# Kernel tuning notes

Hardware: AMD Instinct MI355X
Metric: run time of the kernel (lower is better)

## Reference

```python
import jax, jax.numpy as jnp
import numpy as np

TOPK_INC = 20  # top-k vertices per mention that form a hyperedge (torch.topk(attention_a, 20))
TOPK_OUT = 2   # top-k node reps concatenated into the output (torch.topk(X_score, k=2))


def _indicator_from_rows(att, idx):
    # att: [N, N], idx: [A] int. Rows with idx == 0 are skipped, as in the original loop.
    N = att.shape[0]
    rows = att[idx]                                   # [A, N] gather of attention rows
    _, top = jax.lax.top_k(rows, TOPK_INC)            # [A, TOPK_INC]
    mask = (idx != 0).astype(att.dtype)               # [A]
    vals = jnp.broadcast_to(mask[:, None], top.shape).reshape(-1)
    # scatter-max builds the 0/1 incidence vector (multiple mentions OR together)
    return jnp.zeros((N,), att.dtype).at[top.reshape(-1)].max(vals)  # [N]


def _forward_one(h, att, a_idx, b_idx, spk, W_w, W_b, S_w, S_b):
    # h: [N, H], att: [N, N], spk: [N] (single speaker row since speak_num == 1 -> E = 3)
    a_ind = _indicator_from_rows(att, a_idx)
    b_ind = _indicator_from_rows(att, b_idx)
    Hyper0 = jnp.stack([a_ind, b_ind, spk], axis=0)   # [E, N] binary incidence
    Dv = 1.0 / jnp.sqrt(Hyper0.sum(axis=0) + 1.0)     # sqrt(inverse(diag(Dv) + I)) diagonal, [N]
    De = 1.0 / jnp.sqrt(Hyper0.sum(axis=1))           # sqrt(inverse(diag(De))) diagonal, [E]
    Hyper = Hyper0 @ att                              # [E, N]  (dropout is identity in eval)
    Hyper_att = jax.nn.softmax(Hyper, axis=-1)        # F.softmax over last dim for 2D input
    Hyper_prime = Hyper_att @ h                       # [E, H]
    w = jax.nn.softmax(Hyper_prime @ W_w.T + W_b, axis=0)[:, 0]  # [E]
    # A = diag(Dv) @ Hyper0.T @ diag(w) @ diag(De) @ Hyper @ diag(Dv); X = A @ h.
    # Associate as M @ (K @ h) to avoid materializing the [N, N] matrix A.
    K = (w * De)[:, None] * Hyper * Dv[None, :]       # [E, N]
    M = Hyper0.T * Dv[:, None]                        # [N, E]
    X = M @ (K @ h)                                   # [N, H]
    score = (X @ S_w.T + S_b)[:, 0]                   # [N]
    _, top = jax.lax.top_k(score, TOPK_OUT)           # [2]
    return X[top].reshape(-1)                         # [2*H]


def setup_inputs() -> dict:
    key = jax.random.key(0)
    B, N, H, A = 32, 1024, 768, 8
    ks = jax.random.split(key, 8)
    inp = jax.random.normal(ks[0], (B, N, H), dtype=jnp.float32)
    word_att = jax.random.uniform(ks[1], (B, 1, N, N), dtype=jnp.float32)
    a_idx = jax.random.randint(ks[2], (B, A), 0, N)
    b_idx = jax.random.randint(ks[3], (B, A), 0, N)
    speak_num = jnp.ones((B, 1), dtype=jnp.int64 if jax.config.jax_enable_x64 else jnp.int32)
    speak_all = jax.random.randint(ks[4], (B, 3, N), 0, 2).astype(jnp.float32)
    W_w = jax.random.normal(ks[5], (1, H), dtype=jnp.float32) * (1.0 / np.sqrt(H))
    W_b = jnp.zeros((1,), dtype=jnp.float32)
    score_w = jax.random.normal(ks[6], (1, H), dtype=jnp.float32) * (1.0 / np.sqrt(H))
    score_b = jnp.zeros((1,), dtype=jnp.float32)
    return {"input": inp, "word_att": word_att, "a_idx": a_idx, "b_idx": b_idx,
            "speak_num": speak_num, "speak_all": speak_all,
            "W_w": W_w, "W_b": W_b, "score_w": score_w, "score_b": score_b}


def reference(input, word_att, a_idx, b_idx, speak_num, speak_all, W_w, W_b, score_w, score_b):
    # speak_num is all ones by construction -> exactly one speaker hyperedge per sample (E = 3)
    att = word_att[:, 0]           # [B, N, N]
    spk = speak_all[:, 0]          # [B, N]
    f = jax.vmap(_forward_one, in_axes=(0, 0, 0, 0, 0, None, None, None, None))
    return f(input, att, a_idx, b_idx, spk, W_w, W_b, score_w, score_b)  # [B, 2*H]
```

## Files before the change

### kernel.cpp

```cpp
#include <hip/hip_runtime.h>
#include <math.h>

#define B_ 32
#define N_ 1024
#define H_ 768
#define A_ 8
#define TOPK_ 20
#define CH4_ 32
#define CMAX_ 1280

__device__ __forceinline__ float wsum(float x) {
#pragma unroll
    for (int off = 32; off > 0; off >>= 1) x += __shfl_xor(x, off);
    return x;
}

__global__ __launch_bounds__(1024) void k1_ind(
    const float* __restrict__ att, const int* __restrict__ a_idx,
    const int* __restrict__ b_idx, const float* __restrict__ speak_all,
    float* __restrict__ aind, float* __restrict__ bind,
    float* __restrict__ Dv, float* __restrict__ De,
    float4* __restrict__ comp, int* __restrict__ npadArr)
{
    const int b = blockIdx.x;
    const int tid = threadIdx.x;
    const int w = tid >> 6, lane = tid & 63;
    __shared__ float s_ind[2][N_];
    __shared__ float s_red[3][16];
    __shared__ int wcnt[16];
    __shared__ int woff[17];

    s_ind[0][tid] = 0.f;
    s_ind[1][tid] = 0.f;
    __syncthreads();

    const int which = w >> 3;
    const int r = w & 7;
    const int idx = which ? b_idx[b * A_ + r] : a_idx[b * A_ + r];
    if (idx != 0) {
        const float* row = att + ((size_t)b * N_ + idx) * N_;
        float v[16];
#pragma unroll
        for (int k = 0; k < 16; ++k) v[k] = row[(k << 6) + lane];
        float* dst = s_ind[which];
        for (int t = 0; t < TOPK_; ++t) {
            float bv = v[0]; int bk = 0;
#pragma unroll
            for (int k = 1; k < 16; ++k)
                if (v[k] > bv) { bv = v[k]; bk = k; }
            int bc = (bk << 6) + lane;
#pragma unroll
            for (int off = 32; off > 0; off >>= 1) {
                float ov = __shfl_xor(bv, off);
                int oc = __shfl_xor(bc, off);
                if (ov > bv || (ov == bv && oc < bc)) { bv = ov; bc = oc; }
            }
            if (lane == 0) dst[bc] = 1.f;
            if (lane == (bc & 63)) v[bc >> 6] = -INFINITY;
        }
    }
    __syncthreads();

    const float sa = s_ind[0][tid], sb = s_ind[1][tid];
    const float ss = speak_all[(size_t)b * 3 * N_ + tid];
    aind[b * N_ + tid] = sa;
    bind[b * N_ + tid] = sb;
    Dv[b * N_ + tid] = 1.f / sqrtf(sa + sb + ss + 1.f);

    float p[3] = {sa, sb, ss};
#pragma unroll
    for (int e = 0; e < 3; ++e) {
        float x = wsum(p[e]);
        if (lane == 0) s_red[e][w] = x;
    }

    const bool act = (sa + sb + ss) > 0.f;
    const unsigned long long m = __ballot(act);
    const int wrank = (int)__popcll(m & ((1ull << lane) - 1ull));
    if (lane == 0) wcnt[w] = (int)__popcll(m);
    __syncthreads();
    if (tid == 0) {
        int s = 0;
        for (int i = 0; i < 16; ++i) { woff[i] = s; s += wcnt[i]; }
        woff[16] = s;
        npadArr[b] = (s + 255) & ~255;
    }
    if (tid < 3) {
        float s = 0.f;
        for (int i = 0; i < 16; ++i) s += s_red[tid][i];
        De[b * 3 + tid] = 1.f / sqrtf(s);
    }
    __syncthreads();
    const int nact = woff[16];
    const int npad = (nact + 255) & ~255;
    if (act)
        comp[(size_t)b * CMAX_ + woff[w] + wrank] = make_float4(__int_as_float(tid), sa, sb, ss);
    for (int i = nact + tid; i < npad; i += 1024)
        comp[(size_t)b * CMAX_ + i] = make_float4(__int_as_float(0), 0.f, 0.f, 0.f);
}

__global__ __launch_bounds__(256, 2) void k2_hyper(
    const float* __restrict__ att, const float4* __restrict__ comp,
    const int* __restrict__ npadArr, float* __restrict__ Hyper)
{
    const int b = blockIdx.y;
    const int col0 = blockIdx.x * 32;
    const int t = threadIdx.x;
    const int cx = t & 7, ig = t >> 3;
    __shared__ float4 scomp[1024];
    __shared__ float scr[256 * 13];

    const int npad = npadArr[b];
    for (int i = t; i < npad; i += 256) scomp[i] = comp[(size_t)b * CMAX_ + i];
    __syncthreads();

    float a0x=0,a0y=0,a0z=0,a0w=0, a1x=0,a1y=0,a1z=0,a1w=0, a2x=0,a2y=0,a2z=0,a2w=0;
    const float* bb = att + (size_t)b * N_ * N_ + col0 + cx * 4;

    if (npad > 0) {
        float4 v[8], cw[8];
        int i = ig;
#pragma unroll
        for (int k = 0; k < 8; ++k) {
            const float4 c = scomp[i];
            cw[k] = c;
            v[k] = *(const float4*)(bb + (size_t)__float_as_int(c.x) * N_);
            i += 32;
        }
        while (i < npad) {
#pragma unroll
            for (int k = 0; k < 8; ++k) {
                const float4 cur = v[k];
                const float4 cc = cw[k];
                const float4 nc = scomp[i];
                cw[k] = nc;
                v[k] = *(const float4*)(bb + (size_t)__float_as_int(nc.x) * N_);
                a0x += cc.y*cur.x; a0y += cc.y*cur.y; a0z += cc.y*cur.z; a0w += cc.y*cur.w;
                a1x += cc.z*cur.x; a1y += cc.z*cur.y; a1z += cc.z*cur.z; a1w += cc.z*cur.w;
                a2x += cc.w*cur.x; a2y += cc.w*cur.y; a2z += cc.w*cur.z; a2w += cc.w*cur.w;
                i += 32;
            }
        }
#pragma unroll
        for (int k = 0; k < 8; ++k) {
            const float4 cur = v[k];
            const float4 cc = cw[k];
            a0x += cc.y*cur.x; a0y += cc.y*cur.y; a0z += cc.y*cur.z; a0w += cc.y*cur.w;
            a1x += cc.z*cur.x; a1y += cc.z*cur.y; a1z += cc.z*cur.z; a1w += cc.z*cur.w;
            a2x += cc.w*cur.x; a2y += cc.w*cur.y; a2z += cc.w*cur.z; a2w += cc.w*cur.w;
        }
    }
    __syncthreads();

    float vals[12] = {a0x,a0y,a0z,a0w, a1x,a1y,a1z,a1w, a2x,a2y,a2z,a2w};
#pragma unroll
    for (int k = 0; k < 12; ++k) scr[t * 13 + k] = vals[k];
    __syncthreads();
    for (int s = 16; s > 0; s >>= 1) {
        if (ig < s) {
#pragma unroll
            for (int k = 0; k < 12; ++k)
                scr[t * 13 + k] += scr[(t + s * 8) * 13 + k];
        }
        __syncthreads();
    }
    if (ig == 0) {
#pragma unroll
        for (int e = 0; e < 3; ++e)
#pragma unroll
            for (int j = 0; j < 4; ++j)
                Hyper[(size_t)(b * 3 + e) * N_ + col0 + cx * 4 + j] = scr[t * 13 + e * 4 + j];
    }
}

__global__ __launch_bounds__(192, 2) void k4_ug(
    const float* __restrict__ h, const float* __restrict__ Hyper,
    const float* __restrict__ Dv, float* __restrict__ UGpart)
{
    const int b = blockIdx.y, c = blockIdx.x;
    const int n0 = c * 32;
    const int t = threadIdx.x;
    const int wv = t >> 6, lane = t & 63;
    __shared__ float sH[3 * N_];
    __shared__ float sw6[6][32];
    __shared__ float smz[6];

    for (int i = t; i < 3 * N_ / 4; i += 192)
        ((float4*)sH)[i] = ((const float4*)(Hyper + (size_t)b * 3 * N_))[i];
    __syncthreads();

    {
        const float* He = sH + wv * N_;
        float m = -INFINITY;
        for (int n = lane; n < N_; n += 64) m = fmaxf(m, He[n]);
#pragma unroll
        for (int off = 32; off > 0; off >>= 1) m = fmaxf(m, __shfl_xor(m, off));
        float z = 0.f;
        for (int n = lane; n < N_; n += 64) z += expf(He[n] - m);
        z = wsum(z);
        if (lane == 0) { smz[wv] = m; smz[3 + wv] = 1.f / z; }
    }
    __syncthreads();
    if (t < 96) {
        const int e = t >> 5, r = t & 31;
        const float Hv = sH[e * N_ + n0 + r];
        sw6[e][r] = expf(Hv - smz[e]) * smz[3 + e];
        sw6[3 + e][r] = Hv * Dv[b * N_ + n0 + r];
    }
    __syncthreads();

    float u0x=0,u0y=0,u0z=0,u0w=0, u1x=0,u1y=0,u1z=0,u1w=0, u2x=0,u2y=0,u2z=0,u2w=0;
    float g0x=0,g0y=0,g0z=0,g0w=0, g1x=0,g1y=0,g1z=0,g1w=0, g2x=0,g2y=0,g2z=0,g2w=0;
    const float* base = h + (size_t)b * N_ * H_ + (size_t)n0 * H_ + t * 4;

    float4 v[8];
#pragma unroll
    for (int k = 0; k < 8; ++k) v[k] = *(const float4*)(base + (size_t)k * H_);
#pragma unroll
    for (int r8 = 0; r8 < 32; r8 += 8) {
#pragma unroll
        for (int k = 0; k < 8; ++k) {
            const int r = r8 + k;
            const float4 cur = v[k];
            if (r + 8 < 32) v[k] = *(const float4*)(base + (size_t)(r + 8) * H_);
            const float w0 = sw6[0][r], w1 = sw6[1][r], w2 = sw6[2][r];
            const float g0 = sw6[3][r], g1 = sw6[4][r], g2 = sw6[5][r];
            u0x += w0*cur.x; u0y += w0*cur.y; u0z += w0*cur.z; u0w += w0*cur.w;
            u1x += w1*cur.x; u1y += w1*cur.y; u1z += w1*cur.z; u1w += w1*cur.w;
            u2x += w2*cur.x; u2y += w2*cur.y; u2z += w2*cur.z; u2w += w2*cur.w;
            g0x += g0*cur.x; g0y += g0*cur.y; g0z += g0*cur.z; g0w += g0*cur.w;
            g1x += g1*cur.x; g1y += g1*cur.y; g1z += g1*cur.z; g1w += g1*cur.w;
            g2x += g2*cur.x; g2y += g2*cur.y; g2z += g2*cur.z; g2w += g2*cur.w;
        }
    }
    float* up = UGpart + (size_t)(b * CH4_ + c) * 6 * H_ + t * 4;
    *(float4*)(up)          = make_float4(u0x, u0y, u0z, u0w);
    *(float4*)(up + H_)     = make_float4(u1x, u1y, u1z, u1w);
    *(float4*)(up + 2*H_)   = make_float4(u2x, u2y, u2z, u2w);
    *(float4*)(up + 3*H_)   = make_float4(g0x, g0y, g0z, g0w);
    *(float4*)(up + 4*H_)   = make_float4(g1x, g1y, g1z, g1w);
    *(float4*)(up + 5*H_)   = make_float4(g2x, g2y, g2z, g2w);
}

__global__ __launch_bounds__(256, 2) void k4b_red(
    const float* __restrict__ UGpart, float* __restrict__ U, float* __restrict__ G)
{
    const int gid = blockIdx.x * 256 + threadIdx.x;
    const int b = gid / 1152;
    const int rem = gid % 1152;
    const int s = rem / 192;
    const int col = (rem % 192) * 4;

    const float* p = UGpart + (size_t)b * CH4_ * 6 * H_ + s * H_ + col;
    float4 a0 = make_float4(0,0,0,0), a1 = make_float4(0,0,0,0);
    float4 a2 = make_float4(0,0,0,0), a3 = make_float4(0,0,0,0);
#pragma unroll
    for (int c = 0; c < CH4_; c += 4) {
        const float4 v0 = *(const float4*)(p + (size_t)(c + 0) * 6 * H_);
        const float4 v1 = *(const float4*)(p + (size_t)(c + 1) * 6 * H_);
        const float4 v2 = *(const float4*)(p + (size_t)(c + 2) * 6 * H_);
        const float4 v3 = *(const float4*)(p + (size_t)(c + 3) * 6 * H_);
        a0.x += v0.x; a0.y += v0.y; a0.z += v0.z; a0.w += v0.w;
        a1.x += v1.x; a1.y += v1.y; a1.z += v1.z; a1.w += v1.w;
        a2.x += v2.x; a2.y += v2.y; a2.z += v2.z; a2.w += v2.w;
        a3.x += v3.x; a3.y += v3.y; a3.z += v3.z; a3.w += v3.w;
    }
    const float4 acc = make_float4(a0.x+a1.x+a2.x+a3.x, a0.y+a1.y+a2.y+a3.y,
                                   a0.z+a1.z+a2.z+a3.z, a0.w+a1.w+a2.w+a3.w);
    if (s < 3) *(float4*)(U + ((size_t)(b * 3 + s)) * H_ + col) = acc;
    else       *(float4*)(G + ((size_t)(b * 3 + s - 3)) * H_ + col) = acc;
}

__global__ __launch_bounds__(256) void k5_fin(
    const float* __restrict__ U, const float* __restrict__ G,
    const float* __restrict__ De, const float* __restrict__ Dv,
    const float* __restrict__ aind, const float* __restrict__ bind,
    const float* __restrict__ speak_all,
    const float* __restrict__ W_w, const float* __restrict__ W_b,
    const float* __restrict__ S_w, const float* __restrict__ S_b,
    float* __restrict__ out)
{
    const int b = blockIdx.x, tid = threadIdx.x;
    const int lane = tid & 63, wv = tid >> 6;
    __shared__ float sKh[3 * H_];
    __shared__ float sscore[N_];
    __shared__ float sred[16];
    __shared__ int sidx[4];

    const float* Ub = U + (size_t)b * 3 * H_;
    const float* Gb = G + (size_t)b * 3 * H_;

    float p0 = 0.f, p1 = 0.f, p2 = 0.f;
    for (int j = tid; j < H_; j += 256) {
        const float ww = W_w[j];
        p0 += Ub[j] * ww; p1 += Ub[H_ + j] * ww; p2 += Ub[2 * H_ + j] * ww;
    }
    p0 = wsum(p0); p1 = wsum(p1); p2 = wsum(p2);
    if (lane == 0) { sred[wv * 3 + 0] = p0; sred[wv * 3 + 1] = p1; sred[wv * 3 + 2] = p2; }
    __syncthreads();
    const float wb = W_b[0];
    const float l0 = sred[0] + sred[3] + sred[6] + sred[9]  + wb;
    const float l1 = sred[1] + sred[4] + sred[7] + sred[10] + wb;
    const float l2 = sred[2] + sred[5] + sred[8] + sred[11] + wb;
    const float mx = fmaxf(l0, fmaxf(l1, l2));
    const float e0 = expf(l0 - mx), e1 = expf(l1 - mx), e2 = expf(l2 - mx);
    const float inv = 1.f / (e0 + e1 + e2);
    const float wd0 = e0 * inv * De[b * 3 + 0];
    const float wd1 = e1 * inv * De[b * 3 + 1];
    const float wd2 = e2 * inv * De[b * 3 + 2];
    __syncthreads();

    for (int j = tid; j < H_; j += 256) {
        sKh[j]          = wd0 * Gb[j];
        sKh[H_ + j]     = wd1 * Gb[H_ + j];
        sKh[2 * H_ + j] = wd2 * Gb[2 * H_ + j];
    }
    __syncthreads();

    float q0 = 0.f, q1 = 0.f, q2 = 0.f;
    for (int j = tid; j < H_; j += 256) {
        const float sw2 = S_w[j];
        q0 += sKh[j] * sw2; q1 += sKh[H_ + j] * sw2; q2 += sKh[2 * H_ + j] * sw2;
    }
    q0 = wsum(q0); q1 = wsum(q1); q2 = wsum(q2);
    if (lane == 0) { sred[wv * 3 + 0] = q0; sred[wv * 3 + 1] = q1; sred[wv * 3 + 2] = q2; }
    __syncthreads();
    q0 = sred[0] + sred[3] + sred[6] + sred[9];
    q1 = sred[1] + sred[4] + sred[7] + sred[10];
    q2 = sred[2] + sred[5] + sred[8] + sred[11];

    const float sb0 = S_b[0];
    const float* av = aind + b * N_;
    const float* bv2 = bind + b * N_;
    const float* dv = Dv + b * N_;
    const float* sv = speak_all + (size_t)b * 3 * N_;
    for (int n = tid; n < N_; n += 256)
        sscore[n] = dv[n] * (av[n] * q0 + bv2[n] * q1 + sv[n] * q2) + sb0;
    __syncthreads();

    int r0;
    {
        float best = -INFINITY; int bi = N_;
        for (int n = tid; n < N_; n += 256) {
            const float s = sscore[n];
            if (s > best || (s == best && n < bi)) { best = s; bi = n; }
        }
#pragma unroll
        for (int off = 32; off > 0; off >>= 1) {
            const float ov = __shfl_xor(best, off); const int oi = __shfl_xor(bi, off);
            if (ov > best || (ov == best && oi < bi)) { best = ov; bi = oi; }
        }
        if (lane == 0) { sred[wv] = best; sidx[wv] = bi; }
        __syncthreads();
        float v = -INFINITY; int i = N_;
        for (int k = 0; k < 4; ++k)
            if (sred[k] > v || (sred[k] == v && sidx[k] < i)) { v = sred[k]; i = sidx[k]; }
        r0 = i;
    }
    __syncthreads();
    int r1;
    {
        float best = -INFINITY; int bi = N_;
        for (int n = tid; n < N_; n += 256) {
            if (n == r0) continue;
            const float s = sscore[n];
            if (s > best || (s == best && n < bi)) { best = s; bi = n; }
        }
#pragma unroll
        for (int off = 32; off > 0; off >>= 1) {
            const float ov = __shfl_xor(best, off); const int oi = __shfl_xor(bi, off);
            if (ov > best || (ov == best && oi < bi)) { best = ov; bi = oi; }
        }
        if (lane == 0) { sred[wv] = best; sidx[wv] = bi; }
        __syncthreads();
        float v = -INFINITY; int i = N_;
        for (int k = 0; k < 4; ++k)
            if (sred[k] > v || (sred[k] == v && sidx[k] < i)) { v = sred[k]; i = sidx[k]; }
        r1 = i;
    }

    float* ob = out + (size_t)b * 2 * H_;
    {
        const float d = dv[r0], wa = av[r0], wbn = bv2[r0], wsv = sv[r0];
        for (int j = tid; j < H_; j += 256)
            ob[j] = d * (wa * sKh[j] + wbn * sKh[H_ + j] + wsv * sKh[2 * H_ + j]);
    }
    {
        const float d = dv[r1], wa = av[r1], wbn = bv2[r1], wsv = sv[r1];
        for (int j = tid; j < H_; j += 256)
            ob[H_ + j] = d * (wa * sKh[j] + wbn * sKh[H_ + j] + wsv * sKh[2 * H_ + j]);
    }
}

extern "C" void kernel_launch(void* const* d_in, const int* in_sizes, int n_in,
                              void* d_out, int out_size, void* d_ws, size_t ws_size,
                              hipStream_t stream)
{
    const float* h         = (const float*)d_in[0];
    const float* att       = (const float*)d_in[1];
    const int*   a_idx     = (const int*)d_in[2];
    const int*   b_idx     = (const int*)d_in[3];
    const float* speak_all = (const float*)d_in[5];
    const float* W_w       = (const float*)d_in[6];
    const float* W_b       = (const float*)d_in[7];
    const float* S_w       = (const float*)d_in[8];
    const float* S_b       = (const float*)d_in[9];
    float* out = (float*)d_out;

    float* ws      = (float*)d_ws;
    float* aind    = ws;
    float* bind    = aind + B_ * N_;
    float* Dv      = bind + B_ * N_;
    float* De      = Dv + B_ * N_;
    int*   npadArr = (int*)(De + 128);
    float4* comp   = (float4*)(De + 256);
    float* Hyper   = De + 256 + B_ * CMAX_ * 4;
    float* UGpart  = Hyper + B_ * 3 * N_;
    float* U       = UGpart + (size_t)B_ * CH4_ * 6 * H_;
    float* G       = U + B_ * 3 * H_;

    k1_ind<<<B_, 1024, 0, stream>>>(att, a_idx, b_idx, speak_all, aind, bind, Dv, De, comp, npadArr);
    k2_hyper<<<dim3(32, B_), 256, 0, stream>>>(att, comp, npadArr, Hyper);
    k4_ug<<<dim3(CH4_, B_), 192, 0, stream>>>(h, Hyper, Dv, UGpart);
    k4b_red<<<144, 256, 0, stream>>>(UGpart, U, G);
    k5_fin<<<B_, 256, 0, stream>>>(U, G, De, Dv, aind, bind, speak_all, W_w, W_b, S_w, S_b, out);
}
```

Measured before the change: 82.96 us.

## Fuse Hyper and UG kernels with per-batch atomic barrier, fold reduction into final

Merges the Hyper gather-matvec kernel and the softmax/h-projection kernel into one launch. The 32 blocks of each batch sync through a global atomic counter with spin-wait, so Hyper is computed and consumed in a single kernel. The partial-sum reduction kernel is folded into the final kernel, which reduces UGpart into shared memory. This removes two kernel launches and the U/G round trip. The costs are a simpler non-prefetched gather loop, float3 loads of h, and a spin barrier that relies on all 1024 blocks being co-resident (256 threads, up to 4 per CU), otherwise it can deadlock.

```diff
diff --git a/kernel.cpp b/kernel.cpp
--- a/kernel.cpp
+++ b/kernel.cpp
@@ -6,7 +6,7 @@
 #define H_ 768
 #define A_ 8
 #define TOPK_ 20
-#define CH4_ 32
+#define CH_ 32
 #define CMAX_ 1280
 
 __device__ __forceinline__ float wsum(float x) {
@@ -20,7 +20,7 @@
     const int* __restrict__ b_idx, const float* __restrict__ speak_all,
     float* __restrict__ aind, float* __restrict__ bind,
     float* __restrict__ Dv, float* __restrict__ De,
-    float4* __restrict__ comp, int* __restrict__ npadArr)
+    float4* __restrict__ comp, int* __restrict__ npadArr, int* __restrict__ cnt)
 {
     const int b = blockIdx.x;
     const int tid = threadIdx.x;
@@ -30,6 +30,8 @@
     __shared__ int wcnt[16];
     __shared__ int woff[17];
 
+    if (b == 0 && tid < 64) cnt[tid] = 0;
+
     s_ind[0][tid] = 0.f;
     s_ind[1][tid] = 0.f;
     __syncthreads();
@@ -43,7 +45,7 @@
 #pragma unroll
         for (int k = 0; k < 16; ++k) v[k] = row[(k << 6) + lane];
         float* dst = s_ind[which];
-        for (int t = 0; t < TOPK_; ++t) {
+        for (int t2 = 0; t2 < TOPK_; ++t2) {
             float bv = v[0]; int bk = 0;
 #pragma unroll
             for (int k = 1; k < 16; ++k)
@@ -99,97 +101,73 @@
         comp[(size_t)b * CMAX_ + i] = make_float4(__int_as_float(0), 0.f, 0.f, 0.f);
 }
 
-__global__ __launch_bounds__(256, 2) void k2_hyper(
+__global__ __launch_bounds__(256, 4) void kBC(
     const float* __restrict__ att, const float4* __restrict__ comp,
-    const int* __restrict__ npadArr, float* __restrict__ Hyper)
+    const int* __restrict__ npadArr, const float* __restrict__ h,
+    const float* __restrict__ Dv, float* __restrict__ Hyper,
+    float* __restrict__ UGpart, int* __restrict__ cnt)
 {
-    const int b = blockIdx.y;
-    const int col0 = blockIdx.x * 32;
+    const int w = blockIdx.x;
+    const int b = w >> 5, chunk = w & 31;
     const int t = threadIdx.x;
-    const int cx = t & 7, ig = t >> 3;
     __shared__ float4 scomp[1024];
-    __shared__ float scr[256 * 13];
+    __shared__ float scr[3328];
+    __shared__ float smz[8];
 
     const int npad = npadArr[b];
     for (int i = t; i < npad; i += 256) scomp[i] = comp[(size_t)b * CMAX_ + i];
     __syncthreads();
-
-    float a0x=0,a0y=0,a0z=0,a0w=0, a1x=0,a1y=0,a1z=0,a1w=0, a2x=0,a2y=0,a2z=0,a2w=0;
-    const float* bb = att + (size_t)b * N_ * N_ + col0 + cx * 4;
-
-    if (npad > 0) {
-        float4 v[8], cw[8];
-        int i = ig;
-#pragma unroll
-        for (int k = 0; k < 8; ++k) {
+    const int cx = t & 7, ig = t >> 3;
+    {
+        float a0x=0,a0y=0,a0z=0,a0w=0, a1x=0,a1y=0,a1z=0,a1w=0, a2x=0,a2y=0,a2z=0,a2w=0;
+        const float* bb = att + (size_t)b * N_ * N_ + chunk * 32 + cx * 4;
+#pragma unroll 4
+        for (int i = ig; i < npad; i += 32) {
             const float4 c = scomp[i];
-            cw[k] = c;
-            v[k] = *(const float4*)(bb + (size_t)__float_as_int(c.x) * N_);
-            i += 32;
-        }
-        while (i < npad) {
-#pragma unroll
-            for (int k = 0; k < 8; ++k) {
-                const float4 cur = v[k];
-                const float4 cc = cw[k];
-                const float4 nc = scomp[i];
-                cw[k] = nc;
-                v[k] = *(const float4*)(bb + (size_t)__float_as_int(nc.x) * N_);
-                a0x += cc.y*cur.x; a0y += cc.y*cur.y; a0z += cc.y*cur.z; a0w += cc.y*cur.w;
-                a1x += cc.z*cur.x; a1y += cc.z*cur.y; a1z += cc.z*cur.z; a1w += cc.z*cur.w;
-                a2x += cc.w*cur.x; a2y += cc.w*cur.y; a2z += cc.w*cur.z; a2w += cc.w*cur.w;
-                i += 32;
+            const float4 v = *(const float4*)(bb + (size_t)__float_as_int(c.x) * N_);
+            a0x += c.y*v.x; a0y += c.y*v.y; a0z += c.y*v.z; a0w += c.y*v.w;
+            a1x += c.z*v.x; a1y += c.z*v.y; a1z += c.z*v.z; a1w += c.z*v.w;
+            a2x += c.w*v.x; a2y += c.w*v.y; a2z += c.w*v.z; a2w += c.w*v.w;
+        }
+        __syncthreads();
+        float vals[12] = {a0x,a0y,a0z,a0w, a1x,a1y,a1z,a1w, a2x,a2y,a2z,a2w};
+#pragma unroll
+        for (int k = 0; k < 12; ++k) scr[t * 13 + k] = vals[k];
+        __syncthreads();
+        for (int s2 = 16; s2 > 0; s2 >>= 1) {
+            if (ig < s2) {
+#pragma unroll
+                for (int k = 0; k < 12; ++k)
+                    scr[t * 13 + k] += scr[(t + s2 * 8) * 13 + k];
             }
-        }
-#pragma unroll
-        for (int k = 0; k < 8; ++k) {
-            const float4 cur = v[k];
-            const float4 cc = cw[k];
-            a0x += cc.y*cur.x; a0y += cc.y*cur.y; a0z += cc.y*cur.z; a0w += cc.y*cur.w;
-            a1x += cc.z*cur.x; a1y += cc.z*cur.y; a1z += cc.z*cur.z; a1w += cc.z*cur.w;
-            a2x += cc.w*cur.x; a2y += cc.w*cur.y; a2z += cc.w*cur.z; a2w += cc.w*cur.w;
-        }
-    }
-    __syncthreads();
-
-    float vals[12] = {a0x,a0y,a0z,a0w, a1x,a1y,a1z,a1w, a2x,a2y,a2z,a2w};
-#pragma unroll
-    for (int k = 0; k < 12; ++k) scr[t * 13 + k] = vals[k];
-    __syncthreads();
-    for (int s = 16; s > 0; s >>= 1) {
-        if (ig < s) {
-#pragma unroll
-            for (int k = 0; k < 12; ++k)
-                scr[t * 13 + k] += scr[(t + s * 8) * 13 + k];
-        }
-        __syncthreads();
-    }
-    if (ig == 0) {
-#pragma unroll
-        for (int e = 0; e < 3; ++e)
-#pragma unroll
-            for (int j = 0; j < 4; ++j)
-                Hyper[(size_t)(b * 3 + e) * N_ + col0 + cx * 4 + j] = scr[t * 13 + e * 4 + j];
-    }
-}
-
-__global__ __launch_bounds__(192, 2) void k4_ug(
-    const float* __restrict__ h, const float* __restrict__ Hyper,
-    const float* __restrict__ Dv, float* __restrict__ UGpart)
-{
-    const int b = blockIdx.y, c = blockIdx.x;
-    const int n0 = c * 32;
-    const int t = threadIdx.x;
+            __syncthreads();
+        }
+        if (ig == 0) {
+#pragma unroll
+            for (int e = 0; e < 3; ++e)
+#pragma unroll
+                for (int j = 0; j < 4; ++j)
+                    Hyper[(size_t)(b * 3 + e) * N_ + chunk * 32 + cx * 4 + j] =
+                        scr[t * 13 + e * 4 + j];
+        }
+    }
+    __threadfence();
+    __syncthreads();
+    if (t == 0) atomicAdd(&cnt[b], 1);
+
+    if (t == 0) {
+        while (atomicAdd(&cnt[b], 0) < 32) __builtin_amdgcn_s_sleep(2);
+    }
+    __syncthreads();
+    __threadfence();
+
+    float* sH = (float*)scomp;
+    float* sw6 = scr;
+    for (int i = t; i < 768; i += 256)
+        ((float4*)sH)[i] = ((const float4*)(Hyper + (size_t)b * 3 * N_))[i];
+    __syncthreads();
     const int wv = t >> 6, lane = t & 63;
-    __shared__ float sH[3 * N_];
-    __shared__ float sw6[6][32];
-    __shared__ float smz[6];
-
-    for (int i = t; i < 3 * N_ / 4; i += 192)
-        ((float4*)sH)[i] = ((const float4*)(Hyper + (size_t)b * 3 * N_))[i];
-    __syncthreads();
-
-    {
+    if (wv < 3) {
         const float* He = sH + wv * N_;
         float m = -INFINITY;
         for (int n = lane; n < N_; n += 64) m = fmaxf(m, He[n]);
@@ -198,81 +176,44 @@
         float z = 0.f;
         for (int n = lane; n < N_; n += 64) z += expf(He[n] - m);
         z = wsum(z);
-        if (lane == 0) { smz[wv] = m; smz[3 + wv] = 1.f / z; }
-    }
-    __syncthreads();
+        if (lane == 0) { smz[wv] = m; smz[4 + wv] = 1.f / z; }
+    }
+    __syncthreads();
+    const int n0 = chunk * 32;
     if (t < 96) {
         const int e = t >> 5, r = t & 31;
         const float Hv = sH[e * N_ + n0 + r];
-        sw6[e][r] = expf(Hv - smz[e]) * smz[3 + e];
-        sw6[3 + e][r] = Hv * Dv[b * N_ + n0 + r];
-    }
-    __syncthreads();
-
-    float u0x=0,u0y=0,u0z=0,u0w=0, u1x=0,u1y=0,u1z=0,u1w=0, u2x=0,u2y=0,u2z=0,u2w=0;
-    float g0x=0,g0y=0,g0z=0,g0w=0, g1x=0,g1y=0,g1z=0,g1w=0, g2x=0,g2y=0,g2z=0,g2w=0;
-    const float* base = h + (size_t)b * N_ * H_ + (size_t)n0 * H_ + t * 4;
-
-    float4 v[8];
-#pragma unroll
-    for (int k = 0; k < 8; ++k) v[k] = *(const float4*)(base + (size_t)k * H_);
-#pragma unroll
-    for (int r8 = 0; r8 < 32; r8 += 8) {
-#pragma unroll
-        for (int k = 0; k < 8; ++k) {
-            const int r = r8 + k;
-            const float4 cur = v[k];
-            if (r + 8 < 32) v[k] = *(const float4*)(base + (size_t)(r + 8) * H_);
-            const float w0 = sw6[0][r], w1 = sw6[1][r], w2 = sw6[2][r];
-            const float g0 = sw6[3][r], g1 = sw6[4][r], g2 = sw6[5][r];
-            u0x += w0*cur.x; u0y += w0*cur.y; u0z += w0*cur.z; u0w += w0*cur.w;
-            u1x += w1*cur.x; u1y += w1*cur.y; u1z += w1*cur.z; u1w += w1*cur.w;
-            u2x += w2*cur.x; u2y += w2*cur.y; u2z += w2*cur.z; u2w += w2*cur.w;
-            g0x += g0*cur.x; g0y += g0*cur.y; g0z += g0*cur.z; g0w += g0*cur.w;
-            g1x += g1*cur.x; g1y += g1*cur.y; g1z += g1*cur.z; g1w += g1*cur.w;
-            g2x += g2*cur.x; g2y += g2*cur.y; g2z += g2*cur.z; g2w += g2*cur.w;
-        }
-    }
-    float* up = UGpart + (size_t)(b * CH4_ + c) * 6 * H_ + t * 4;
-    *(float4*)(up)          = make_float4(u0x, u0y, u0z, u0w);
-    *(float4*)(up + H_)     = make_float4(u1x, u1y, u1z, u1w);
-    *(float4*)(up + 2*H_)   = make_float4(u2x, u2y, u2z, u2w);
-    *(float4*)(up + 3*H_)   = make_float4(g0x, g0y, g0z, g0w);
-    *(float4*)(up + 4*H_)   = make_float4(g1x, g1y, g1z, g1w);
-    *(float4*)(up + 5*H_)   = make_float4(g2x, g2y, g2z, g2w);
-}
-
-__global__ __launch_bounds__(256, 2) void k4b_red(
-    const float* __restrict__ UGpart, float* __restrict__ U, float* __restrict__ G)
-{
-    const int gid = blockIdx.x * 256 + threadIdx.x;
-    const int b = gid / 1152;
-    const int rem = gid % 1152;
-    const int s = rem / 192;
-    const int col = (rem % 192) * 4;
-
-    const float* p = UGpart + (size_t)b * CH4_ * 6 * H_ + s * H_ + col;
-    float4 a0 = make_float4(0,0,0,0), a1 = make_float4(0,0,0,0);
-    float4 a2 = make_float4(0,0,0,0), a3 = make_float4(0,0,0,0);
-#pragma unroll
-    for (int c = 0; c < CH4_; c += 4) {
-        const float4 v0 = *(const float4*)(p + (size_t)(c + 0) * 6 * H_);
-        const float4 v1 = *(const float4*)(p + (size_t)(c + 1) * 6 * H_);
-        const float4 v2 = *(const float4*)(p + (size_t)(c + 2) * 6 * H_);
-        const float4 v3 = *(const float4*)(p + (size_t)(c + 3) * 6 * H_);
-        a0.x += v0.x; a0.y += v0.y; a0.z += v0.z; a0.w += v0.w;
-        a1.x += v1.x; a1.y += v1.y; a1.z += v1.z; a1.w += v1.w;
-        a2.x += v2.x; a2.y += v2.y; a2.z += v2.z; a2.w += v2.w;
-        a3.x += v3.x; a3.y += v3.y; a3.z += v3.z; a3.w += v3.w;
-    }
-    const float4 acc = make_float4(a0.x+a1.x+a2.x+a3.x, a0.y+a1.y+a2.y+a3.y,
-                                   a0.z+a1.z+a2.z+a3.z, a0.w+a1.w+a2.w+a3.w);
-    if (s < 3) *(float4*)(U + ((size_t)(b * 3 + s)) * H_ + col) = acc;
-    else       *(float4*)(G + ((size_t)(b * 3 + s - 3)) * H_ + col) = acc;
-}
-
-__global__ __launch_bounds__(256) void k5_fin(
-    const float* __restrict__ U, const float* __restrict__ G,
+        sw6[e * 32 + r] = expf(Hv - smz[e]) * smz[4 + e];
+        sw6[96 + e * 32 + r] = Hv * Dv[b * N_ + n0 + r];
+    }
+    __syncthreads();
+
+    float u00=0,u01=0,u02=0, u10=0,u11=0,u12=0, u20=0,u21=0,u22=0;
+    float g00=0,g01=0,g02=0, g10=0,g11=0,g12=0, g20=0,g21=0,g22=0;
+    const float* base = h + (size_t)b * N_ * H_ + (size_t)n0 * H_ + t * 3;
+#pragma unroll 8
+    for (int r = 0; r < 32; ++r) {
+        const float3 v = *(const float3*)(base + (size_t)r * H_);
+        const float w0 = sw6[r], w1 = sw6[32 + r], w2 = sw6[64 + r];
+        const float g0 = sw6[96 + r], g1 = sw6[128 + r], g2 = sw6[160 + r];
+        u00 += w0*v.x; u01 += w0*v.y; u02 += w0*v.z;
+        u10 += w1*v.x; u11 += w1*v.y; u12 += w1*v.z;
+        u20 += w2*v.x; u21 += w2*v.y; u22 += w2*v.z;
+        g00 += g0*v.x; g01 += g0*v.y; g02 += g0*v.z;
+        g10 += g1*v.x; g11 += g1*v.y; g12 += g1*v.z;
+        g20 += g2*v.x; g21 += g2*v.y; g22 += g2*v.z;
+    }
+    float* up = UGpart + (size_t)(b * CH_ + chunk) * 6 * H_ + t * 3;
+    up[0] = u00; up[1] = u01; up[2] = u02;
+    up[H_ + 0] = u10; up[H_ + 1] = u11; up[H_ + 2] = u12;
+    up[2*H_ + 0] = u20; up[2*H_ + 1] = u21; up[2*H_ + 2] = u22;
+    up[3*H_ + 0] = g00; up[3*H_ + 1] = g01; up[3*H_ + 2] = g02;
+    up[4*H_ + 0] = g10; up[4*H_ + 1] = g11; up[4*H_ + 2] = g12;
+    up[5*H_ + 0] = g20; up[5*H_ + 1] = g21; up[5*H_ + 2] = g22;
+}
+
+__global__ __launch_bounds__(256) void k45_fin(
+    const float* __restrict__ UGpart,
     const float* __restrict__ De, const float* __restrict__ Dv,
     const float* __restrict__ aind, const float* __restrict__ bind,
     const float* __restrict__ speak_all,
@@ -282,13 +223,39 @@
 {
     const int b = blockIdx.x, tid = threadIdx.x;
     const int lane = tid & 63, wv = tid >> 6;
+    __shared__ float sUG[6 * H_];
     __shared__ float sKh[3 * H_];
     __shared__ float sscore[N_];
     __shared__ float sred[16];
     __shared__ int sidx[4];
 
-    const float* Ub = U + (size_t)b * 3 * H_;
-    const float* Gb = G + (size_t)b * 3 * H_;
+    {
+        const float* p = UGpart + (size_t)b * CH_ * 6 * H_;
+        for (int slot = tid; slot < 1152; slot += 256) {
+            const int off = slot * 4;
+            float4 a0 = make_float4(0,0,0,0), a1 = make_float4(0,0,0,0);
+            float4 a2 = make_float4(0,0,0,0), a3 = make_float4(0,0,0,0);
+#pragma unroll
+            for (int c = 0; c < CH_; c += 4) {
+                const float4 v0 = *(const float4*)(p + (size_t)(c + 0) * 6 * H_ + off);
+                const float4 v1 = *(const float4*)(p + (size_t)(c + 1) * 6 * H_ + off);
+                const float4 v2 = *(const float4*)(p + (size_t)(c + 2) * 6 * H_ + off);
+                const float4 v3 = *(const float4*)(p + (size_t)(c + 3) * 6 * H_ + off);
+                a0.x += v0.x; a0.y += v0.y; a0.z += v0.z; a0.w += v0.w;
+                a1.x += v1.x; a1.y += v1.y; a1.z += v1.z; a1.w += v1.w;
+                a2.x += v2.x; a2.y += v2.y; a2.z += v2.z; a2.w += v2.w;
+                a3.x += v3.x; a3.y += v3.y; a3.z += v3.z; a3.w += v3.w;
+            }
+            sUG[off + 0] = a0.x + a1.x + a2.x + a3.x;
+            sUG[off + 1] = a0.y + a1.y + a2.y + a3.y;
+            sUG[off + 2] = a0.z + a1.z + a2.z + a3.z;
+            sUG[off + 3] = a0.w + a1.w + a2.w + a3.w;
+        }
+    }
+    __syncthreads();
+
+    const float* Ub = sUG;
+    const float* Gb = sUG + 3 * H_;
 
     float p0 = 0.f, p1 = 0.f, p2 = 0.f;
     for (int j = tid; j < H_; j += 256) {
@@ -413,15 +380,14 @@
     float* Dv      = bind + B_ * N_;
     float* De      = Dv + B_ * N_;
     int*   npadArr = (int*)(De + 128);
-    float4* comp   = (float4*)(De + 256);
-    float* Hyper   = De + 256 + B_ * CMAX_ * 4;
+    int*   cnt     = npadArr + 64;
+    float4* comp   = (float4*)(npadArr + 128);
+    float* Hyper   = (float*)(comp + (size_t)B_ * CMAX_);
     float* UGpart  = Hyper + B_ * 3 * N_;
-    float* U       = UGpart + (size_t)B_ * CH4_ * 6 * H_;
-    float* G       = U + B_ * 3 * H_;
-
-    k1_ind<<<B_, 1024, 0, stream>>>(att, a_idx, b_idx, speak_all, aind, bind, Dv, De, comp, npadArr);
-    k2_hyper<<<dim3(32, B_), 256, 0, stream>>>(att, comp, npadArr, Hyper);
-    k4_ug<<<dim3(CH4_, B_), 192, 0, stream>>>(h, Hyper, Dv, UGpart);
-    k4b_red<<<144, 256, 0, stream>>>(UGpart, U, G);
-    k5_fin<<<B_, 256, 0, stream>>>(U, G, De, Dv, aind, bind, speak_all, W_w, W_b, S_w, S_b, out);
-}
+
+    k1_ind<<<B_, 1024, 0, stream>>>(att, a_idx, b_idx, speak_all, aind, bind,
+                                    Dv, De, comp, npadArr, cnt);
+    kBC<<<B_ * CH_, 256, 0, stream>>>(att, comp, npadArr, h, Dv, Hyper, UGpart, cnt);
+    k45_fin<<<B_, 256, 0, stream>>>(UGpart, De, Dv, aind, bind, speak_all,
+                                    W_w, W_b, S_w, S_b, out);
+}
```

Result: slower. 258.2 us (+211.2%).
